# Performance work log

Hardware: AMD Instinct MI355X
Metric: run time of the kernel (lower is better)

## Reference

```python
import jax, jax.numpy as jnp
import numpy as np
import math

B, N, M = 128, 16, 32
D_OBS, D_OUT = 128, 128            # obs_input_dim, obs_output_dim (== obs_output_dim_other)
D_OA, D_AV = 136, 128              # obs_act_input_dim, obs_act_output_dim
D_OBS_O, D_OA_O, D_AV_O = 128, 136, 128
D_FINAL_IN, D_HID, D_FINAL_OUT = 256, 64, 1
N_ACT = 8


def setup_inputs() -> dict:
    key = jax.random.key(0)
    ks = jax.random.split(key, 16)
    s = 0.05
    return {
        "states": jax.random.normal(ks[0], (B, N, D_OBS), jnp.float32),
        "policies": jax.random.uniform(ks[1], (B, N, N_ACT), jnp.float32),
        "actions": jax.random.uniform(ks[2], (B, N, N_ACT), jnp.float32),
        "states_other": jax.random.normal(ks[3], (B, M, D_OBS_O), jnp.float32),
        "actions_other": jax.random.uniform(ks[4], (B, M, N_ACT), jnp.float32),
        # weights stored as [in, out] (torch Linear applies x @ W.T)
        "Wk": jax.random.normal(ks[5], (D_OBS, D_OUT), jnp.float32) * s,
        "Wq": jax.random.normal(ks[6], (D_OBS, D_OUT), jnp.float32) * s,
        "Wv": jax.random.normal(ks[7], (D_OA, D_AV), jnp.float32) * s,
        "Wk_o": jax.random.normal(ks[8], (D_OBS_O, D_OUT), jnp.float32) * s,
        "Wq_o": jax.random.normal(ks[9], (D_OBS, D_OUT), jnp.float32) * s,
        "Wv_o": jax.random.normal(ks[10], (D_OA_O, D_AV_O), jnp.float32) * s,
        "W1": jax.random.normal(ks[11], (D_FINAL_IN, D_HID), jnp.float32) * s,
        "W2": jax.random.normal(ks[12], (D_HID, D_FINAL_OUT), jnp.float32) * s,
    }


def reference(states, policies, actions, states_other, actions_other,
              Wk, Wq, Wv, Wk_o, Wq_o, Wv_o, W1, W2):
    d_k = float(D_OUT)
    d_k_o = float(D_OUT)  # d_k_obs_other = obs_output_dim_other

    obs_actions = jnp.concatenate([states, actions], axis=-1)   # [B,N,D_OA]
    obs_policy = jnp.concatenate([states, policies], axis=-1)   # [B,N,D_OA]

    k = states @ Wk                                             # [B,N,D_OUT]
    q = states @ Wq
    score = jnp.einsum('bid,bjd->bij', q, k)                    # [B,N,N]
    # torch softmaxes over the key axis (after reshape gymnastics)
    weight = jax.nn.softmax(score / math.sqrt(d_k), axis=-1)    # [B,N,N]
    ret_weight = weight

    # oap[b,j,k] = obs_policy[b,k] if j==k else obs_actions[b,k]
    eye = jnp.eye(N, dtype=states.dtype)[None, :, :, None]      # [1,N,N,1]
    oap = eye * obs_policy[:, None, :, :] + (1.0 - eye) * obs_actions[:, None, :, :]  # [B,N,N,D_OA]
    av = jnp.tanh(oap @ Wv)                                     # [B,N(j),N(k),D_AV]

    # torch: repeat av over a new agent axis i, multiply by weight[b,i,k], sum over k
    wav = jnp.einsum('bik,bjkd->bijd', weight, av)              # [B,N,N,D_AV]

    obs_actions_other = jnp.concatenate([states_other, actions_other], axis=-1)  # [B,M,D_OA_O]
    k_o = states_other @ Wk_o                                   # [B,M,D_OUT]
    q_o = states @ Wq_o                                         # [B,N,D_OUT]
    av_o = jnp.tanh(obs_actions_other @ Wv_o)                   # [B,M,D_AV_O]

    score_o = jnp.einsum('bid,bmd->bim', q_o, k_o)              # [B,N,M]
    # torch softmax dim=-2: over the agent axis (faithful, even if unusual)
    weight_o = jax.nn.softmax(score_o / math.sqrt(d_k_o), axis=1)  # [B,N,M]
    wav_o = jnp.einsum('bim,bmd->bid', weight_o, av_o)          # [B,N,D_AV_O]
    wav_o_b = jnp.broadcast_to(wav_o[:, :, None, :], (wav_o.shape[0], N, N, D_AV_O))

    node = jnp.concatenate([wav, wav_o_b], axis=-1)             # [B,N,N,256]
    h = jax.nn.leaky_relu(node @ W1)                            # [B,N,N,64]
    value = h @ W2                                              # [B,N,N,1]
    return value, ret_weight, weight_o[..., None]
```

## Files before the change

### kernel.cpp

```cpp
#include <hip/hip_runtime.h>
#include <math.h>

#define NB   128
#define NN   16
#define MM   32
#define DD   128
#define NACT 8
#define HH   64

#define OFF_G   0
#define OFF_GO  16384
#define OFF_Q   32768
#define OFF_QO  (OFF_Q  + NB*NN*DD)
#define OFF_P   (OFF_QO + NB*NN*DD)
#define OFF_PO  (OFF_P  + NB*NN*HH)
#define OFF_V   (OFF_PO + NB*MM*HH)
#define WS_FLOATS (OFF_V + NB*NN*HH)

__device__ float g_ws[WS_FLOATS];

__launch_bounds__(256)
__global__ void k0_gram(const float* __restrict__ Wq,  const float* __restrict__ Wk,
                        const float* __restrict__ Wqo, const float* __restrict__ Wko) {
    __shared__ float sA[16 * 129];
    __shared__ float sB[16 * 129];
    const int blk = blockIdx.x;
    const int mat = blk >> 6;
    const int tile = blk & 63;
    const int r0 = (tile >> 3) * 16, c0 = (tile & 7) * 16;
    const float* A  = mat ? Wqo : Wq;
    const float* Bm = mat ? Wko : Wk;
    float* outp = g_ws + (mat ? OFF_GO : OFF_G);
    const int t = threadIdx.x;
    for (int idx = t; idx < 16 * 128; idx += 256) {
        int r = idx >> 7, c = idx & 127;
        sA[r * 129 + c] = A [(r0 + r) * 128 + c];
        sB[r * 129 + c] = Bm[(c0 + r) * 128 + c];
    }
    __syncthreads();
    const int r = t >> 4, c = t & 15;
    float acc = 0.f;
    #pragma unroll 8
    for (int o = 0; o < 128; ++o) acc += sA[r * 129 + o] * sB[c * 129 + o];
    outp[(r0 + r) * 128 + (c0 + c)] = acc;
}

#define AVO_P 132
__launch_bounds__(512)
__global__ void k1_proj(const float* __restrict__ states,   const float* __restrict__ policies,
                        const float* __restrict__ actions,  const float* __restrict__ states_o,
                        const float* __restrict__ actions_o,
                        const float* __restrict__ Wv, const float* __restrict__ Wvo,
                        const float* __restrict__ W1) {
    __shared__ float sm[4096 + 256 + 32 * AVO_P];
    const int bs = blockIdx.x >> 1;
    const int side = blockIdx.x & 1;
    const int t = threadIdx.x;

    if (side == 0) {
        float* s_st = sm;
        float* s_ac = sm + 2048;
        float* s_po = sm + 2176;
        float* s_aa = sm + 2304;
        float* s_ap = sm + 4352;
        ((float4*)s_st)[t] = ((const float4*)(states + bs * NN * DD))[t];
        if (t < NN * NACT) {
            s_ac[t] = actions [bs * NN * NACT + t];
            s_po[t] = policies[bs * NN * NACT + t];
        }
        __syncthreads();
        {
            const int g = t >> 7, c = t & 127;
            float q4[4] = {0,0,0,0}, qo4[4] = {0,0,0,0}, av4[4] = {0,0,0,0};
            const float* G  = g_ws + OFF_G;
            const float* Go = g_ws + OFF_GO;
            for (int kk = 0; kk < DD; ++kk) {
                float wg = G[kk * 128 + c], wgo = Go[kk * 128 + c], wv = Wv[kk * 128 + c];
                #pragma unroll
                for (int u = 0; u < 4; ++u) {
                    float x = s_st[(g + 4 * u) * 128 + kk];
                    q4[u] += x * wg; qo4[u] += x * wgo; av4[u] += x * wv;
                }
            }
            float aa[4], ap[4];
            #pragma unroll
            for (int u = 0; u < 4; ++u) { aa[u] = av4[u]; ap[u] = av4[u]; }
            for (int kk = 0; kk < NACT; ++kk) {
                float wv = Wv[(DD + kk) * 128 + c];
                #pragma unroll
                for (int u = 0; u < 4; ++u) {
                    aa[u] += s_ac[(g + 4 * u) * NACT + kk] * wv;
                    ap[u] += s_po[(g + 4 * u) * NACT + kk] * wv;
                }
            }
            #pragma unroll
            for (int u = 0; u < 4; ++u) {
                int row = g + 4 * u;
                g_ws[OFF_Q  + bs * 2048 + row * 128 + c] = q4[u];
                g_ws[OFF_QO + bs * 2048 + row * 128 + c] = qo4[u];
                s_aa[row * 128 + c] = tanhf(aa[u]);
                s_ap[row * 128 + c] = tanhf(ap[u]);
            }
        }
        __syncthreads();
        {
            const int i = t >> 5, h2 = (t & 31) * 2;
            float p0 = 0.f, p1 = 0.f, v0 = 0.f, v1 = 0.f;
            for (int kk = 0; kk < DD; ++kk) {
                float2 w = *(const float2*)(W1 + kk * HH + h2);
                float a = s_aa[i * 128 + kk];
                float d = s_ap[i * 128 + kk] - a;
                p0 += a * w.x; p1 += a * w.y;
                v0 += d * w.x; v1 += d * w.y;
            }
            *(float2*)(g_ws + OFF_P + bs * NN * HH + i * HH + h2) = make_float2(p0, p1);
            *(float2*)(g_ws + OFF_V + bs * NN * HH + i * HH + h2) = make_float2(v0, v1);
        }
    } else {
        float* s_so = sm;
        float* s_ao = sm + 4096;
        float* s_av = sm + 4352;
        ((float4*)s_so)[t]       = ((const float4*)(states_o + bs * MM * DD))[t];
        ((float4*)s_so)[t + 512] = ((const float4*)(states_o + bs * MM * DD))[t + 512];
        if (t < MM * NACT) s_ao[t] = actions_o[bs * MM * NACT + t];
        __syncthreads();
        {
            const int g = t >> 7, c = t & 127;
            float av8[8] = {0,0,0,0,0,0,0,0};
            for (int kk = 0; kk < DD; ++kk) {
                float wvo = Wvo[kk * 128 + c];
                #pragma unroll
                for (int u = 0; u < 8; ++u) av8[u] += s_so[(g + 4 * u) * 128 + kk] * wvo;
            }
            for (int kk = 0; kk < NACT; ++kk) {
                float wvo = Wvo[(DD + kk) * 128 + c];
                #pragma unroll
                for (int u = 0; u < 8; ++u) av8[u] += s_ao[(g + 4 * u) * NACT + kk] * wvo;
            }
            #pragma unroll
            for (int u = 0; u < 8; ++u) s_av[(g + 4 * u) * AVO_P + c] = tanhf(av8[u]);
        }
        __syncthreads();
        {
            const int r = t >> 4, h4 = (t & 15) * 4;
            float4 acc = {0.f, 0.f, 0.f, 0.f};
            for (int kk = 0; kk < DD; ++kk) {
                float4 w = *(const float4*)(W1 + (DD + kk) * HH + h4);
                float a = s_av[r * AVO_P + kk];
                acc.x += a * w.x; acc.y += a * w.y; acc.z += a * w.z; acc.w += a * w.w;
            }
            *(float4*)(g_ws + OFF_PO + bs * MM * HH + r * HH + h4) = acc;
        }
    }
}

__launch_bounds__(512)
__global__ void k2_attn(const float* __restrict__ states, const float* __restrict__ states_o,
                        const float* __restrict__ W2, float* __restrict__ out) {
    __shared__ float s_q [16 * 129];
    __shared__ float s_qo[16 * 129];
    __shared__ float s_st[16 * 129];
    __shared__ float s_so[32 * 129];
    __shared__ float s_P [16 * 64];
    __shared__ float s_Po[32 * 64];
    __shared__ float s_V [16 * 65];
    __shared__ float s_U [16 * 65];
    __shared__ float s_w [16 * 17];
    __shared__ float s_wo[16 * 33];
    __shared__ float s_W2[64];
    const int b = blockIdx.x, t = threadIdx.x;

    for (int idx = t; idx < NN * DD; idx += 512) {
        int r = idx >> 7, d = idx & 127;
        s_q [r * 129 + d] = g_ws[OFF_Q  + b * 2048 + idx];
        s_qo[r * 129 + d] = g_ws[OFF_QO + b * 2048 + idx];
        s_st[r * 129 + d] = states[b * 2048 + idx];
    }
    for (int idx = t; idx < MM * DD; idx += 512) {
        int r = idx >> 7, d = idx & 127;
        s_so[r * 129 + d] = states_o[b * 4096 + idx];
    }
    if (t < 256) ((float4*)s_P)[t] = ((const float4*)(g_ws + OFF_P + b * NN * HH))[t];
    ((float4*)s_Po)[t] = ((const float4*)(g_ws + OFF_PO + b * MM * HH))[t];
    for (int idx = t; idx < NN * HH; idx += 512) {
        int r = idx >> 6, h = idx & 63;
        s_V[r * 65 + h] = g_ws[OFF_V + b * NN * HH + idx];
    }
    if (t < HH) s_W2[t] = W2[t];
    __syncthreads();

    const float scale = 0.08838834764831845f;
    {
        int i = t >> 5, m = t & 31;
        float acc = 0.f;
        #pragma unroll 8
        for (int d = 0; d < DD; ++d) acc += s_qo[i * 129 + d] * s_so[m * 129 + d];
        s_wo[i * 33 + m] = acc * scale;
    }
    if (t < 256) {
        int i = t >> 4, j = t & 15;
        float acc = 0.f;
        #pragma unroll 8
        for (int d = 0; d < DD; ++d) acc += s_q[i * 129 + d] * s_st[j * 129 + d];
        s_w[i * 17 + j] = acc * scale;
    }
    __syncthreads();

    if (t < NN) {
        int i = t;
        float mx = -1e30f;
        #pragma unroll
        for (int j = 0; j < NN; ++j) mx = fmaxf(mx, s_w[i * 17 + j]);
        float e[NN], sum = 0.f;
        #pragma unroll
        for (int j = 0; j < NN; ++j) { e[j] = expf(s_w[i * 17 + j] - mx); sum += e[j]; }
        float inv = 1.f / sum;
        #pragma unroll
        for (int j = 0; j < NN; ++j) s_w[i * 17 + j] = e[j] * inv;
    } else if (t >= 64 && t < 64 + MM) {
        int m = t - 64;
        float mx = -1e30f;
        #pragma unroll
        for (int i = 0; i < NN; ++i) mx = fmaxf(mx, s_wo[i * 33 + m]);
        float e[NN], sum = 0.f;
        #pragma unroll
        for (int i = 0; i < NN; ++i) { e[i] = expf(s_wo[i * 33 + m] - mx); sum += e[i]; }
        float inv = 1.f / sum;
        #pragma unroll
        for (int i = 0; i < NN; ++i) s_wo[i * 33 + m] = e[i] * inv;
    }
    __syncthreads();

    if (t < NN * NN) out[NB * 256 + b * 256 + t] = s_w[(t >> 4) * 17 + (t & 15)];
    out[2 * NB * 256 + b * 512 + t] = s_wo[(t >> 5) * 33 + (t & 31)];

    {
        int i = t >> 5, h2 = (t & 31) * 2;
        float u0 = 0.f, u1 = 0.f;
        #pragma unroll
        for (int k = 0; k < NN; ++k) {
            float w = s_w[i * 17 + k];
            u0 += w * s_P[k * 64 + h2];
            u1 += w * s_P[k * 64 + h2 + 1];
        }
        #pragma unroll
        for (int m = 0; m < MM; ++m) {
            float w = s_wo[i * 33 + m];
            u0 += w * s_Po[m * 64 + h2];
            u1 += w * s_Po[m * 64 + h2 + 1];
        }
        s_U[i * 65 + h2]     = u0;
        s_U[i * 65 + h2 + 1] = u1;
    }
    __syncthreads();

    if (t < NN * NN) {
        int i = t >> 4, j = t & 15;
        float wij = s_w[i * 17 + j];
        float acc = 0.f;
        #pragma unroll
        for (int h = 0; h < HH; ++h) {
            float x = s_U[i * 65 + h] + wij * s_V[j * 65 + h];
            x = (x > 0.f) ? x : 0.01f * x;
            acc += x * s_W2[h];
        }
        out[b * 256 + t] = acc;
    }
}

extern "C" void kernel_launch(void* const* d_in, const int* in_sizes, int n_in,
                              void* d_out, int out_size, void* d_ws, size_t ws_size,
                              hipStream_t stream) {
    const float* states    = (const float*)d_in[0];
    const float* policies  = (const float*)d_in[1];
    const float* actions   = (const float*)d_in[2];
    const float* states_o  = (const float*)d_in[3];
    const float* actions_o = (const float*)d_in[4];
    const float* Wk        = (const float*)d_in[5];
    const float* Wq        = (const float*)d_in[6];
    const float* Wv        = (const float*)d_in[7];
    const float* Wk_o      = (const float*)d_in[8];
    const float* Wq_o      = (const float*)d_in[9];
    const float* Wv_o      = (const float*)d_in[10];
    const float* W1        = (const float*)d_in[11];
    const float* W2        = (const float*)d_in[12];
    float* out = (float*)d_out;

    hipLaunchKernelGGL(k0_gram, dim3(128), dim3(256), 0, stream, Wq, Wk, Wq_o, Wk_o);
    hipLaunchKernelGGL(k1_proj, dim3(256), dim3(512), 0, stream,
                       states, policies, actions, states_o, actions_o, Wv, Wv_o, W1);
    hipLaunchKernelGGL(k2_attn, dim3(128), dim3(512), 0, stream, states, states_o, W2, out);
}
```

Measured before the change: 118.0 us.

## Split projection and attention into row-tiled GEMM kernels with more blocks

Replaces the per-batch projection kernel (256 blocks) with a 32-row-tiled GEMM kernel over flattened rows (1280 blocks), adds a second kernel that does the W1 projections and both attention score matmuls across 768 blocks, and leaves a light final kernel for the softmaxes and value output. The aim is to expose far more parallelism on a GPU with many CUs, where the old 128/256-block grids underfilled the device. In exchange, intermediates (aa, diff, av_o, scores) now round-trip through global memory and there is one extra kernel launch.

```diff
diff --git a/kernel.cpp b/kernel.cpp
--- a/kernel.cpp
+++ b/kernel.cpp
@@ -1,21 +1,26 @@
 #include <hip/hip_runtime.h>
 #include <math.h>
 
-#define NB   128
-#define NN   16
-#define MM   32
-#define DD   128
+#define NB 128
+#define NN 16
+#define MM 32
+#define DD 128
 #define NACT 8
-#define HH   64
+#define HH 64
 
 #define OFF_G   0
 #define OFF_GO  16384
 #define OFF_Q   32768
-#define OFF_QO  (OFF_Q  + NB*NN*DD)
-#define OFF_P   (OFF_QO + NB*NN*DD)
-#define OFF_PO  (OFF_P  + NB*NN*HH)
-#define OFF_V   (OFF_PO + NB*MM*HH)
-#define WS_FLOATS (OFF_V + NB*NN*HH)
+#define OFF_QO  (OFF_Q  + 2048*128)
+#define OFF_AA  (OFF_QO + 2048*128)
+#define OFF_DF  (OFF_AA + 2048*128)
+#define OFF_AVO (OFF_DF + 2048*128)
+#define OFF_P   (OFF_AVO + 4096*128)
+#define OFF_V   (OFF_P  + 2048*64)
+#define OFF_PO  (OFF_V  + 2048*64)
+#define OFF_S   (OFF_PO + 4096*64)
+#define OFF_SO  (OFF_S  + 128*256)
+#define WS_FLOATS (OFF_SO + 128*512)
 
 __device__ float g_ws[WS_FLOATS];
 
@@ -45,222 +50,258 @@
     outp[(r0 + r) * 128 + (c0 + c)] = acc;
 }
 
-#define AVO_P 132
-__launch_bounds__(512)
-__global__ void k1_proj(const float* __restrict__ states,   const float* __restrict__ policies,
-                        const float* __restrict__ actions,  const float* __restrict__ states_o,
-                        const float* __restrict__ actions_o,
-                        const float* __restrict__ Wv, const float* __restrict__ Wvo,
-                        const float* __restrict__ W1) {
-    __shared__ float sm[4096 + 256 + 32 * AVO_P];
-    const int bs = blockIdx.x >> 1;
-    const int side = blockIdx.x & 1;
+__launch_bounds__(256)
+__global__ void k_proj(const float* __restrict__ states,   const float* __restrict__ policies,
+                       const float* __restrict__ actions,  const float* __restrict__ states_o,
+                       const float* __restrict__ actions_o,
+                       const float* __restrict__ Wv, const float* __restrict__ Wvo) {
+    __shared__ float AT[128][34];
+    __shared__ float s_c1[32][NACT];
+    __shared__ float s_c2[32][NACT];
     const int t = threadIdx.x;
-
-    if (side == 0) {
-        float* s_st = sm;
-        float* s_ac = sm + 2048;
-        float* s_po = sm + 2176;
-        float* s_aa = sm + 2304;
-        float* s_ap = sm + 4352;
-        ((float4*)s_st)[t] = ((const float4*)(states + bs * NN * DD))[t];
-        if (t < NN * NACT) {
-            s_ac[t] = actions [bs * NN * NACT + t];
-            s_po[t] = policies[bs * NN * NACT + t];
+    const int tx = t & 15, ty = t >> 4;
+    const int blk = blockIdx.x;
+
+    const float* Asrc; const float* Bsrc; float* dst;
+    int bcol, mode, r0;
+    if (blk < 768) {
+        int rt = blk / 12, ct = blk % 12;
+        r0 = rt * 32;
+        Asrc = states + r0 * 128;
+        if (ct < 4)      { Bsrc = g_ws + OFF_G;  bcol = ct * 32;       dst = g_ws + OFF_Q  + r0 * 128; mode = 0; }
+        else if (ct < 8) { Bsrc = g_ws + OFF_GO; bcol = (ct - 4) * 32; dst = g_ws + OFF_QO + r0 * 128; mode = 0; }
+        else             { Bsrc = Wv;            bcol = (ct - 8) * 32; dst = g_ws + OFF_AA + r0 * 128; mode = 1; }
+    } else {
+        int tile = blk - 768;
+        int rt = tile >> 2, ct = tile & 3;
+        r0 = rt * 32;
+        Asrc = states_o + r0 * 128;
+        Bsrc = Wvo; bcol = ct * 32; dst = g_ws + OFF_AVO + r0 * 128; mode = 2;
+    }
+
+    #pragma unroll
+    for (int u = 0; u < 4; ++u) {
+        int f4 = t + u * 256;
+        int row = f4 >> 5, c4 = (f4 & 31) * 4;
+        float4 v = *(const float4*)(Asrc + row * 128 + c4);
+        AT[c4 + 0][row] = v.x; AT[c4 + 1][row] = v.y;
+        AT[c4 + 2][row] = v.z; AT[c4 + 3][row] = v.w;
+    }
+    {
+        int row = t >> 3, k = t & 7;
+        if (mode == 1) {
+            s_c1[row][k] = actions [(r0 + row) * NACT + k];
+            s_c2[row][k] = policies[(r0 + row) * NACT + k];
+        } else if (mode == 2) {
+            s_c1[row][k] = actions_o[(r0 + row) * NACT + k];
+        }
+    }
+    __syncthreads();
+
+    const int cc = bcol + 2 * tx;
+    float a00 = 0.f, a01 = 0.f, a10 = 0.f, a11 = 0.f;
+    #pragma unroll 8
+    for (int kk = 0; kk < 128; ++kk) {
+        float2 a  = *(const float2*)&AT[kk][2 * ty];
+        float2 bv = *(const float2*)(Bsrc + kk * 128 + cc);
+        a00 += a.x * bv.x; a01 += a.x * bv.y;
+        a10 += a.y * bv.x; a11 += a.y * bv.y;
+    }
+
+    if (mode == 0) {
+        *(float2*)(dst + (2 * ty)     * 128 + cc) = make_float2(a00, a01);
+        *(float2*)(dst + (2 * ty + 1) * 128 + cc) = make_float2(a10, a11);
+    } else if (mode == 1) {
+        float aa00 = a00, aa01 = a01, aa10 = a10, aa11 = a11;
+        float ap00 = a00, ap01 = a01, ap10 = a10, ap11 = a11;
+        #pragma unroll
+        for (int k = 0; k < NACT; ++k) {
+            float2 w = *(const float2*)(Wv + (128 + k) * 128 + cc);
+            float c1a = s_c1[2 * ty][k], c1b = s_c1[2 * ty + 1][k];
+            float c2a = s_c2[2 * ty][k], c2b = s_c2[2 * ty + 1][k];
+            aa00 += c1a * w.x; aa01 += c1a * w.y; aa10 += c1b * w.x; aa11 += c1b * w.y;
+            ap00 += c2a * w.x; ap01 += c2a * w.y; ap10 += c2b * w.x; ap11 += c2b * w.y;
+        }
+        aa00 = tanhf(aa00); aa01 = tanhf(aa01); aa10 = tanhf(aa10); aa11 = tanhf(aa11);
+        ap00 = tanhf(ap00); ap01 = tanhf(ap01); ap10 = tanhf(ap10); ap11 = tanhf(ap11);
+        float* ddf = g_ws + OFF_DF + r0 * 128;
+        *(float2*)(dst + (2 * ty)     * 128 + cc) = make_float2(aa00, aa01);
+        *(float2*)(dst + (2 * ty + 1) * 128 + cc) = make_float2(aa10, aa11);
+        *(float2*)(ddf + (2 * ty)     * 128 + cc) = make_float2(ap00 - aa00, ap01 - aa01);
+        *(float2*)(ddf + (2 * ty + 1) * 128 + cc) = make_float2(ap10 - aa10, ap11 - aa11);
+    } else {
+        #pragma unroll
+        for (int k = 0; k < NACT; ++k) {
+            float2 w = *(const float2*)(Wvo + (128 + k) * 128 + cc);
+            float c1a = s_c1[2 * ty][k], c1b = s_c1[2 * ty + 1][k];
+            a00 += c1a * w.x; a01 += c1a * w.y; a10 += c1b * w.x; a11 += c1b * w.y;
+        }
+        *(float2*)(dst + (2 * ty)     * 128 + cc) = make_float2(tanhf(a00), tanhf(a01));
+        *(float2*)(dst + (2 * ty + 1) * 128 + cc) = make_float2(tanhf(a10), tanhf(a11));
+    }
+}
+
+__launch_bounds__(256)
+__global__ void k_w1(const float* __restrict__ states, const float* __restrict__ states_o,
+                     const float* __restrict__ W1) {
+    __shared__ float smem[6336];
+    const int blk = blockIdx.x, t = threadIdx.x;
+    const float scale = 0.08838834764831845f;
+
+    if (blk < 512) {
+        const int rt = blk >> 1, ct = blk & 1;
+        const int fr = rt * 32;
+        const float* Asrc; const float* Bsrc; float* dst;
+        if (fr < 2048)      { Asrc = g_ws + OFF_AA  + fr * 128;          Bsrc = W1;            dst = g_ws + OFF_P  + fr * 64; }
+        else if (fr < 4096) { Asrc = g_ws + OFF_DF  + (fr - 2048) * 128; Bsrc = W1;            dst = g_ws + OFF_V  + (fr - 2048) * 64; }
+        else                { Asrc = g_ws + OFF_AVO + (fr - 4096) * 128; Bsrc = W1 + 128 * 64; dst = g_ws + OFF_PO + (fr - 4096) * 64; }
+        #pragma unroll
+        for (int u = 0; u < 4; ++u) {
+            int f4 = t + u * 256;
+            int row = f4 >> 5, c4 = (f4 & 31) * 4;
+            float4 v = *(const float4*)(Asrc + row * 128 + c4);
+            smem[(c4 + 0) * 34 + row] = v.x; smem[(c4 + 1) * 34 + row] = v.y;
+            smem[(c4 + 2) * 34 + row] = v.z; smem[(c4 + 3) * 34 + row] = v.w;
         }
         __syncthreads();
-        {
-            const int g = t >> 7, c = t & 127;
-            float q4[4] = {0,0,0,0}, qo4[4] = {0,0,0,0}, av4[4] = {0,0,0,0};
-            const float* G  = g_ws + OFF_G;
-            const float* Go = g_ws + OFF_GO;
-            for (int kk = 0; kk < DD; ++kk) {
-                float wg = G[kk * 128 + c], wgo = Go[kk * 128 + c], wv = Wv[kk * 128 + c];
-                #pragma unroll
-                for (int u = 0; u < 4; ++u) {
-                    float x = s_st[(g + 4 * u) * 128 + kk];
-                    q4[u] += x * wg; qo4[u] += x * wgo; av4[u] += x * wv;
-                }
-            }
-            float aa[4], ap[4];
-            #pragma unroll
-            for (int u = 0; u < 4; ++u) { aa[u] = av4[u]; ap[u] = av4[u]; }
-            for (int kk = 0; kk < NACT; ++kk) {
-                float wv = Wv[(DD + kk) * 128 + c];
-                #pragma unroll
-                for (int u = 0; u < 4; ++u) {
-                    aa[u] += s_ac[(g + 4 * u) * NACT + kk] * wv;
-                    ap[u] += s_po[(g + 4 * u) * NACT + kk] * wv;
-                }
-            }
-            #pragma unroll
-            for (int u = 0; u < 4; ++u) {
-                int row = g + 4 * u;
-                g_ws[OFF_Q  + bs * 2048 + row * 128 + c] = q4[u];
-                g_ws[OFF_QO + bs * 2048 + row * 128 + c] = qo4[u];
-                s_aa[row * 128 + c] = tanhf(aa[u]);
-                s_ap[row * 128 + c] = tanhf(ap[u]);
-            }
+        const int tx = t & 15, ty = t >> 4;
+        const int cc = ct * 32 + 2 * tx;
+        float a00 = 0.f, a01 = 0.f, a10 = 0.f, a11 = 0.f;
+        #pragma unroll 8
+        for (int kk = 0; kk < 128; ++kk) {
+            float2 a  = *(const float2*)&smem[kk * 34 + 2 * ty];
+            float2 bv = *(const float2*)(Bsrc + kk * 64 + cc);
+            a00 += a.x * bv.x; a01 += a.x * bv.y;
+            a10 += a.y * bv.x; a11 += a.y * bv.y;
+        }
+        *(float2*)(dst + (2 * ty)     * 64 + cc) = make_float2(a00, a01);
+        *(float2*)(dst + (2 * ty + 1) * 64 + cc) = make_float2(a10, a11);
+    } else if (blk < 640) {
+        const int b = blk - 512;
+        float* sq  = smem;
+        float* sst = smem + 2112;
+        #pragma unroll
+        for (int u = 0; u < 2; ++u) {
+            int f4 = t + u * 256;
+            int row = f4 >> 5, c4 = (f4 & 31) * 4;
+            *(float4*)&sq [row * 132 + c4] = *(const float4*)(g_ws + OFF_Q + (b * 16 + row) * 128 + c4);
+            *(float4*)&sst[row * 132 + c4] = *(const float4*)(states      + (b * 16 + row) * 128 + c4);
         }
         __syncthreads();
-        {
-            const int i = t >> 5, h2 = (t & 31) * 2;
-            float p0 = 0.f, p1 = 0.f, v0 = 0.f, v1 = 0.f;
-            for (int kk = 0; kk < DD; ++kk) {
-                float2 w = *(const float2*)(W1 + kk * HH + h2);
-                float a = s_aa[i * 128 + kk];
-                float d = s_ap[i * 128 + kk] - a;
-                p0 += a * w.x; p1 += a * w.y;
-                v0 += d * w.x; v1 += d * w.y;
-            }
-            *(float2*)(g_ws + OFF_P + bs * NN * HH + i * HH + h2) = make_float2(p0, p1);
-            *(float2*)(g_ws + OFF_V + bs * NN * HH + i * HH + h2) = make_float2(v0, v1);
-        }
+        const int i = t >> 4, j = t & 15;
+        float acc = 0.f;
+        #pragma unroll 8
+        for (int d = 0; d < 128; ++d) acc += sq[i * 132 + d] * sst[j * 132 + d];
+        g_ws[OFF_S + b * 256 + t] = acc * scale;
     } else {
-        float* s_so = sm;
-        float* s_ao = sm + 4096;
-        float* s_av = sm + 4352;
-        ((float4*)s_so)[t]       = ((const float4*)(states_o + bs * MM * DD))[t];
-        ((float4*)s_so)[t + 512] = ((const float4*)(states_o + bs * MM * DD))[t + 512];
-        if (t < MM * NACT) s_ao[t] = actions_o[bs * MM * NACT + t];
+        const int b = blk - 640;
+        float* sq  = smem;
+        float* sso = smem + 2112;
+        #pragma unroll
+        for (int u = 0; u < 2; ++u) {
+            int f4 = t + u * 256;
+            int row = f4 >> 5, c4 = (f4 & 31) * 4;
+            *(float4*)&sq[row * 132 + c4] = *(const float4*)(g_ws + OFF_QO + (b * 16 + row) * 128 + c4);
+        }
+        #pragma unroll
+        for (int u = 0; u < 4; ++u) {
+            int f4 = t + u * 256;
+            int row = f4 >> 5, c4 = (f4 & 31) * 4;
+            *(float4*)&sso[row * 132 + c4] = *(const float4*)(states_o + (b * 32 + row) * 128 + c4);
+        }
         __syncthreads();
-        {
-            const int g = t >> 7, c = t & 127;
-            float av8[8] = {0,0,0,0,0,0,0,0};
-            for (int kk = 0; kk < DD; ++kk) {
-                float wvo = Wvo[kk * 128 + c];
-                #pragma unroll
-                for (int u = 0; u < 8; ++u) av8[u] += s_so[(g + 4 * u) * 128 + kk] * wvo;
-            }
-            for (int kk = 0; kk < NACT; ++kk) {
-                float wvo = Wvo[(DD + kk) * 128 + c];
-                #pragma unroll
-                for (int u = 0; u < 8; ++u) av8[u] += s_ao[(g + 4 * u) * NACT + kk] * wvo;
-            }
-            #pragma unroll
-            for (int u = 0; u < 8; ++u) s_av[(g + 4 * u) * AVO_P + c] = tanhf(av8[u]);
-        }
-        __syncthreads();
-        {
-            const int r = t >> 4, h4 = (t & 15) * 4;
-            float4 acc = {0.f, 0.f, 0.f, 0.f};
-            for (int kk = 0; kk < DD; ++kk) {
-                float4 w = *(const float4*)(W1 + (DD + kk) * HH + h4);
-                float a = s_av[r * AVO_P + kk];
-                acc.x += a * w.x; acc.y += a * w.y; acc.z += a * w.z; acc.w += a * w.w;
-            }
-            *(float4*)(g_ws + OFF_PO + bs * MM * HH + r * HH + h4) = acc;
-        }
-    }
-}
-
-__launch_bounds__(512)
-__global__ void k2_attn(const float* __restrict__ states, const float* __restrict__ states_o,
-                        const float* __restrict__ W2, float* __restrict__ out) {
-    __shared__ float s_q [16 * 129];
-    __shared__ float s_qo[16 * 129];
-    __shared__ float s_st[16 * 129];
-    __shared__ float s_so[32 * 129];
+        const int m = t & 31, i0 = t >> 5;
+        float acc0 = 0.f, acc1 = 0.f;
+        #pragma unroll 8
+        for (int d = 0; d < 128; ++d) {
+            float s = sso[m * 132 + d];
+            acc0 += sq[i0 * 132 + d] * s;
+            acc1 += sq[(i0 + 8) * 132 + d] * s;
+        }
+        g_ws[OFF_SO + b * 512 + i0 * 32 + m]       = acc0 * scale;
+        g_ws[OFF_SO + b * 512 + (i0 + 8) * 32 + m] = acc1 * scale;
+    }
+}
+
+__launch_bounds__(256)
+__global__ void k2_fin(const float* __restrict__ W2, float* __restrict__ out) {
+    __shared__ float s_w [16][17];
+    __shared__ float s_wo[16][33];
     __shared__ float s_P [16 * 64];
     __shared__ float s_Po[32 * 64];
-    __shared__ float s_V [16 * 65];
-    __shared__ float s_U [16 * 65];
-    __shared__ float s_w [16 * 17];
-    __shared__ float s_wo[16 * 33];
+    __shared__ float s_V [16][65];
+    __shared__ float s_U [16][65];
     __shared__ float s_W2[64];
     const int b = blockIdx.x, t = threadIdx.x;
 
-    for (int idx = t; idx < NN * DD; idx += 512) {
-        int r = idx >> 7, d = idx & 127;
-        s_q [r * 129 + d] = g_ws[OFF_Q  + b * 2048 + idx];
-        s_qo[r * 129 + d] = g_ws[OFF_QO + b * 2048 + idx];
-        s_st[r * 129 + d] = states[b * 2048 + idx];
-    }
-    for (int idx = t; idx < MM * DD; idx += 512) {
-        int r = idx >> 7, d = idx & 127;
-        s_so[r * 129 + d] = states_o[b * 4096 + idx];
-    }
-    if (t < 256) ((float4*)s_P)[t] = ((const float4*)(g_ws + OFF_P + b * NN * HH))[t];
-    ((float4*)s_Po)[t] = ((const float4*)(g_ws + OFF_PO + b * MM * HH))[t];
-    for (int idx = t; idx < NN * HH; idx += 512) {
-        int r = idx >> 6, h = idx & 63;
-        s_V[r * 65 + h] = g_ws[OFF_V + b * NN * HH + idx];
-    }
-    if (t < HH) s_W2[t] = W2[t];
-    __syncthreads();
-
-    const float scale = 0.08838834764831845f;
-    {
-        int i = t >> 5, m = t & 31;
-        float acc = 0.f;
-        #pragma unroll 8
-        for (int d = 0; d < DD; ++d) acc += s_qo[i * 129 + d] * s_so[m * 129 + d];
-        s_wo[i * 33 + m] = acc * scale;
-    }
-    if (t < 256) {
-        int i = t >> 4, j = t & 15;
-        float acc = 0.f;
-        #pragma unroll 8
-        for (int d = 0; d < DD; ++d) acc += s_q[i * 129 + d] * s_st[j * 129 + d];
-        s_w[i * 17 + j] = acc * scale;
-    }
-    __syncthreads();
-
-    if (t < NN) {
-        int i = t;
+    s_w[t >> 4][t & 15] = g_ws[OFF_S + b * 256 + t];
+    s_wo[t >> 5][t & 31]            = g_ws[OFF_SO + b * 512 + t];
+    s_wo[(t + 256) >> 5][t & 31]    = g_ws[OFF_SO + b * 512 + 256 + t];
+    ((float4*)s_P)[t] = ((const float4*)(g_ws + OFF_P + b * 1024))[t];
+    ((float4*)s_Po)[t]       = ((const float4*)(g_ws + OFF_PO + b * 2048))[t];
+    ((float4*)s_Po)[t + 256] = ((const float4*)(g_ws + OFF_PO + b * 2048))[t + 256];
+    #pragma unroll
+    for (int u = 0; u < 4; ++u) {
+        int idx = t + u * 256;
+        s_V[idx >> 6][idx & 63] = g_ws[OFF_V + b * 1024 + idx];
+    }
+    if (t < 64) s_W2[t] = W2[t];
+    __syncthreads();
+
+    if (t < 16) {
         float mx = -1e30f;
         #pragma unroll
-        for (int j = 0; j < NN; ++j) mx = fmaxf(mx, s_w[i * 17 + j]);
+        for (int j = 0; j < NN; ++j) mx = fmaxf(mx, s_w[t][j]);
         float e[NN], sum = 0.f;
         #pragma unroll
-        for (int j = 0; j < NN; ++j) { e[j] = expf(s_w[i * 17 + j] - mx); sum += e[j]; }
+        for (int j = 0; j < NN; ++j) { e[j] = expf(s_w[t][j] - mx); sum += e[j]; }
         float inv = 1.f / sum;
         #pragma unroll
-        for (int j = 0; j < NN; ++j) s_w[i * 17 + j] = e[j] * inv;
-    } else if (t >= 64 && t < 64 + MM) {
+        for (int j = 0; j < NN; ++j) s_w[t][j] = e[j] * inv;
+    } else if (t >= 64 && t < 96) {
         int m = t - 64;
         float mx = -1e30f;
         #pragma unroll
-        for (int i = 0; i < NN; ++i) mx = fmaxf(mx, s_wo[i * 33 + m]);
+        for (int i = 0; i < NN; ++i) mx = fmaxf(mx, s_wo[i][m]);
         float e[NN], sum = 0.f;
         #pragma unroll
-        for (int i = 0; i < NN; ++i) { e[i] = expf(s_wo[i * 33 + m] - mx); sum += e[i]; }
+        for (int i = 0; i < NN; ++i) { e[i] = expf(s_wo[i][m] - mx); sum += e[i]; }
         float inv = 1.f / sum;
         #pragma unroll
-        for (int i = 0; i < NN; ++i) s_wo[i * 33 + m] = e[i] * inv;
-    }
-    __syncthreads();
-
-    if (t < NN * NN) out[NB * 256 + b * 256 + t] = s_w[(t >> 4) * 17 + (t & 15)];
-    out[2 * NB * 256 + b * 512 + t] = s_wo[(t >> 5) * 33 + (t & 31)];
+        for (int i = 0; i < NN; ++i) s_wo[i][m] = e[i] * inv;
+    }
+    __syncthreads();
+
+    out[NB * 256 + b * 256 + t] = s_w[t >> 4][t & 15];
+    out[2 * NB * 256 + b * 512 + t]       = s_wo[t >> 5][t & 31];
+    out[2 * NB * 256 + b * 512 + 256 + t] = s_wo[(t + 256) >> 5][t & 31];
 
     {
-        int i = t >> 5, h2 = (t & 31) * 2;
-        float u0 = 0.f, u1 = 0.f;
+        int i = t >> 4, h0 = (t & 15) * 4;
+        float u0 = 0.f, u1 = 0.f, u2 = 0.f, u3 = 0.f;
         #pragma unroll
         for (int k = 0; k < NN; ++k) {
-            float w = s_w[i * 17 + k];
-            u0 += w * s_P[k * 64 + h2];
-            u1 += w * s_P[k * 64 + h2 + 1];
+            float w = s_w[i][k];
+            float4 p = *(const float4*)&s_P[k * 64 + h0];
+            u0 += w * p.x; u1 += w * p.y; u2 += w * p.z; u3 += w * p.w;
         }
         #pragma unroll
         for (int m = 0; m < MM; ++m) {
-            float w = s_wo[i * 33 + m];
-            u0 += w * s_Po[m * 64 + h2];
-            u1 += w * s_Po[m * 64 + h2 + 1];
-        }
-        s_U[i * 65 + h2]     = u0;
-        s_U[i * 65 + h2 + 1] = u1;
-    }
-    __syncthreads();
-
-    if (t < NN * NN) {
+            float w = s_wo[i][m];
+            float4 p = *(const float4*)&s_Po[m * 64 + h0];
+            u0 += w * p.x; u1 += w * p.y; u2 += w * p.z; u3 += w * p.w;
+        }
+        s_U[i][h0] = u0; s_U[i][h0 + 1] = u1; s_U[i][h0 + 2] = u2; s_U[i][h0 + 3] = u3;
+    }
+    __syncthreads();
+
+    {
         int i = t >> 4, j = t & 15;
-        float wij = s_w[i * 17 + j];
+        float wij = s_w[i][j];
         float acc = 0.f;
         #pragma unroll
         for (int h = 0; h < HH; ++h) {
-            float x = s_U[i * 65 + h] + wij * s_V[j * 65 + h];
+            float x = s_U[i][h] + wij * s_V[j][h];
             x = (x > 0.f) ? x : 0.01f * x;
             acc += x * s_W2[h];
         }
@@ -286,8 +327,9 @@
     const float* W2        = (const float*)d_in[12];
     float* out = (float*)d_out;
 
-    hipLaunchKernelGGL(k0_gram, dim3(128), dim3(256), 0, stream, Wq, Wk, Wq_o, Wk_o);
-    hipLaunchKernelGGL(k1_proj, dim3(256), dim3(512), 0, stream,
-                       states, policies, actions, states_o, actions_o, Wv, Wv_o, W1);
-    hipLaunchKernelGGL(k2_attn, dim3(128), dim3(512), 0, stream, states, states_o, W2, out);
-}
+    hipLaunchKernelGGL(k0_gram, dim3(128),  dim3(256), 0, stream, Wq, Wk, Wq_o, Wk_o);
+    hipLaunchKernelGGL(k_proj,  dim3(1280), dim3(256), 0, stream,
+                       states, policies, actions, states_o, actions_o, Wv, Wv_o);
+    hipLaunchKernelGGL(k_w1,    dim3(768),  dim3(256), 0, stream, states, states_o, W1);
+    hipLaunchKernelGGL(k2_fin,  dim3(128),  dim3(256), 0, stream, W2, out);
+}
```

After: 124.5 us. 5.5% more time.

## Fuse projections and attention per side, drop Gram precompute kernel

Applied to the files above, without the earlier changes.

Replaces the three-kernel pipeline (Gram matrix precompute, projection, attention) with two kernels. The first kernel computes Q, K and V directly on each side (self and other) and finishes attention scores, softmax and the W1 partial products in the same block. The second kernel only combines the partial U and V terms into the final value. This removes one launch, the Gram precompute and the global round trips of Q/Qo and states, and it uses float4 weight loads. In exchange it recomputes K projections per batch instead of folding them into a Gram matrix, and the self and other sides now carry unequal amounts of work.

```diff
diff --git a/kernel.cpp b/kernel.cpp
--- a/kernel.cpp
+++ b/kernel.cpp
@@ -1,271 +1,259 @@
 #include <hip/hip_runtime.h>
 #include <math.h>
 
-#define NB   128
-#define NN   16
-#define MM   32
-#define DD   128
+#define NB 128
+#define NN 16
+#define MM 32
+#define DD 128
 #define NACT 8
-#define HH   64
-
-#define OFF_G   0
-#define OFF_GO  16384
-#define OFF_Q   32768
-#define OFF_QO  (OFF_Q  + NB*NN*DD)
-#define OFF_P   (OFF_QO + NB*NN*DD)
-#define OFF_PO  (OFF_P  + NB*NN*HH)
-#define OFF_V   (OFF_PO + NB*MM*HH)
-#define WS_FLOATS (OFF_V + NB*NN*HH)
+#define HH 64
+
+#define WS_W  0
+#define WS_V  32768
+#define WS_US 163840
+#define WS_UO 294912
+#define WS_FLOATS (WS_UO + 131072)
 
 __device__ float g_ws[WS_FLOATS];
 
-__launch_bounds__(256)
-__global__ void k0_gram(const float* __restrict__ Wq,  const float* __restrict__ Wk,
-                        const float* __restrict__ Wqo, const float* __restrict__ Wko) {
-    __shared__ float sA[16 * 129];
-    __shared__ float sB[16 * 129];
-    const int blk = blockIdx.x;
-    const int mat = blk >> 6;
-    const int tile = blk & 63;
-    const int r0 = (tile >> 3) * 16, c0 = (tile & 7) * 16;
-    const float* A  = mat ? Wqo : Wq;
-    const float* Bm = mat ? Wko : Wk;
-    float* outp = g_ws + (mat ? OFF_GO : OFF_G);
-    const int t = threadIdx.x;
-    for (int idx = t; idx < 16 * 128; idx += 256) {
-        int r = idx >> 7, c = idx & 127;
-        sA[r * 129 + c] = A [(r0 + r) * 128 + c];
-        sB[r * 129 + c] = Bm[(c0 + r) * 128 + c];
-    }
-    __syncthreads();
-    const int r = t >> 4, c = t & 15;
-    float acc = 0.f;
-    #pragma unroll 8
-    for (int o = 0; o < 128; ++o) acc += sA[r * 129 + o] * sB[c * 129 + o];
-    outp[(r0 + r) * 128 + (c0 + c)] = acc;
-}
-
-#define AVO_P 132
-__launch_bounds__(512)
-__global__ void k1_proj(const float* __restrict__ states,   const float* __restrict__ policies,
+#define A_ST 0
+#define A_Q  2112
+#define A_K  4224
+#define A_AA 6336
+#define A_DF 8448
+#define A_P  10560
+#define A_W  11648
+#define A_AC 11920
+#define A_PO 12048
+#define B_ST  0
+#define B_STO 2112
+#define B_QO  6336
+#define B_KOT 8448
+#define B_AVO 12672
+#define B_PO  16896
+#define B_WO  19072
+#define B_AO  19600
+#define SM_FLOATS 19856
+
+__device__ __forceinline__ float4 tanh4(float4 v) {
+    float4 r; r.x = tanhf(v.x); r.y = tanhf(v.y); r.z = tanhf(v.z); r.w = tanhf(v.w); return r;
+}
+__device__ __forceinline__ void fma4(float4& a, float s, const float4& w) {
+    a.x += s * w.x; a.y += s * w.y; a.z += s * w.z; a.w += s * w.w;
+}
+
+__launch_bounds__(512, 1)
+__global__ void k_sides(const float* __restrict__ states,   const float* __restrict__ policies,
                         const float* __restrict__ actions,  const float* __restrict__ states_o,
                         const float* __restrict__ actions_o,
-                        const float* __restrict__ Wv, const float* __restrict__ Wvo,
-                        const float* __restrict__ W1) {
-    __shared__ float sm[4096 + 256 + 32 * AVO_P];
-    const int bs = blockIdx.x >> 1;
+                        const float* __restrict__ Wq,  const float* __restrict__ Wk,
+                        const float* __restrict__ Wv,  const float* __restrict__ Wqo,
+                        const float* __restrict__ Wko, const float* __restrict__ Wvo,
+                        const float* __restrict__ W1,
+                        float* __restrict__ out) {
+    __shared__ float sm[SM_FLOATS];
+    const int b = blockIdx.x >> 1;
     const int side = blockIdx.x & 1;
     const int t = threadIdx.x;
+    const float scale = 0.08838834764831845f;
 
     if (side == 0) {
-        float* s_st = sm;
-        float* s_ac = sm + 2048;
-        float* s_po = sm + 2176;
-        float* s_aa = sm + 2304;
-        float* s_ap = sm + 4352;
-        ((float4*)s_st)[t] = ((const float4*)(states + bs * NN * DD))[t];
-        if (t < NN * NACT) {
-            s_ac[t] = actions [bs * NN * NACT + t];
-            s_po[t] = policies[bs * NN * NACT + t];
-        }
-        __syncthreads();
-        {
-            const int g = t >> 7, c = t & 127;
-            float q4[4] = {0,0,0,0}, qo4[4] = {0,0,0,0}, av4[4] = {0,0,0,0};
-            const float* G  = g_ws + OFF_G;
-            const float* Go = g_ws + OFF_GO;
-            for (int kk = 0; kk < DD; ++kk) {
-                float wg = G[kk * 128 + c], wgo = Go[kk * 128 + c], wv = Wv[kk * 128 + c];
-                #pragma unroll
-                for (int u = 0; u < 4; ++u) {
-                    float x = s_st[(g + 4 * u) * 128 + kk];
-                    q4[u] += x * wg; qo4[u] += x * wgo; av4[u] += x * wv;
-                }
-            }
-            float aa[4], ap[4];
-            #pragma unroll
-            for (int u = 0; u < 4; ++u) { aa[u] = av4[u]; ap[u] = av4[u]; }
+        {
+            int row = t >> 5, c4 = (t & 31) * 4;
+            *(float4*)&sm[A_ST + row * 132 + c4] = *(const float4*)(states + b * 2048 + row * 128 + c4);
+            if (t < 128) sm[A_AC + t] = actions [b * 128 + t];
+            else if (t < 256) sm[A_PO + (t - 128)] = policies[b * 128 + (t - 128)];
+        }
+        __syncthreads();
+        {
+            const int i = t >> 5, c4 = (t & 31) * 4;
+            float4 aq = {0,0,0,0}, ak = {0,0,0,0}, av = {0,0,0,0};
+            #pragma unroll 4
+            for (int kk = 0; kk < DD; ++kk) {
+                float x = sm[A_ST + i * 132 + kk];
+                fma4(aq, x, *(const float4*)(Wq + kk * 128 + c4));
+                fma4(ak, x, *(const float4*)(Wk + kk * 128 + c4));
+                fma4(av, x, *(const float4*)(Wv + kk * 128 + c4));
+            }
+            float4 aa = av, ap = av;
+            #pragma unroll
             for (int kk = 0; kk < NACT; ++kk) {
-                float wv = Wv[(DD + kk) * 128 + c];
-                #pragma unroll
-                for (int u = 0; u < 4; ++u) {
-                    aa[u] += s_ac[(g + 4 * u) * NACT + kk] * wv;
-                    ap[u] += s_po[(g + 4 * u) * NACT + kk] * wv;
-                }
-            }
-            #pragma unroll
-            for (int u = 0; u < 4; ++u) {
-                int row = g + 4 * u;
-                g_ws[OFF_Q  + bs * 2048 + row * 128 + c] = q4[u];
-                g_ws[OFF_QO + bs * 2048 + row * 128 + c] = qo4[u];
-                s_aa[row * 128 + c] = tanhf(aa[u]);
-                s_ap[row * 128 + c] = tanhf(ap[u]);
-            }
-        }
-        __syncthreads();
-        {
-            const int i = t >> 5, h2 = (t & 31) * 2;
-            float p0 = 0.f, p1 = 0.f, v0 = 0.f, v1 = 0.f;
-            for (int kk = 0; kk < DD; ++kk) {
-                float2 w = *(const float2*)(W1 + kk * HH + h2);
-                float a = s_aa[i * 128 + kk];
-                float d = s_ap[i * 128 + kk] - a;
-                p0 += a * w.x; p1 += a * w.y;
-                v0 += d * w.x; v1 += d * w.y;
-            }
-            *(float2*)(g_ws + OFF_P + bs * NN * HH + i * HH + h2) = make_float2(p0, p1);
-            *(float2*)(g_ws + OFF_V + bs * NN * HH + i * HH + h2) = make_float2(v0, v1);
+                float4 wv = *(const float4*)(Wv + (DD + kk) * 128 + c4);
+                fma4(aa, sm[A_AC + i * NACT + kk], wv);
+                fma4(ap, sm[A_PO + i * NACT + kk], wv);
+            }
+            aa = tanh4(aa); ap = tanh4(ap);
+            float4 df; df.x = ap.x - aa.x; df.y = ap.y - aa.y; df.z = ap.z - aa.z; df.w = ap.w - aa.w;
+            *(float4*)&sm[A_Q  + i * 132 + c4] = aq;
+            *(float4*)&sm[A_K  + i * 132 + c4] = ak;
+            *(float4*)&sm[A_AA + i * 132 + c4] = aa;
+            *(float4*)&sm[A_DF + i * 132 + c4] = df;
+        }
+        __syncthreads();
+        if (t < 256) {
+            int i = t >> 4, j = t & 15;
+            float acc = 0.f;
+            #pragma unroll 8
+            for (int d = 0; d < DD; ++d) acc += sm[A_Q + i * 132 + d] * sm[A_K + j * 132 + d];
+            sm[A_W + i * 17 + j] = acc * scale;
+        } else {
+            int tt = t - 256, i = tt >> 4, h4 = (tt & 15) * 4;
+            float4 accp = {0,0,0,0}, accv = {0,0,0,0};
+            #pragma unroll 4
+            for (int kk = 0; kk < DD; ++kk) {
+                float4 w4 = *(const float4*)(W1 + kk * HH + h4);
+                fma4(accp, sm[A_AA + i * 132 + kk], w4);
+                fma4(accv, sm[A_DF + i * 132 + kk], w4);
+            }
+            *(float4*)&sm[A_P + i * 68 + h4] = accp;
+            *(float4*)(g_ws + WS_V + b * 1024 + i * 64 + h4) = accv;
+        }
+        __syncthreads();
+        if (t < NN) {
+            float mx = -1e30f;
+            #pragma unroll
+            for (int j = 0; j < NN; ++j) mx = fmaxf(mx, sm[A_W + t * 17 + j]);
+            float e[NN], sum = 0.f;
+            #pragma unroll
+            for (int j = 0; j < NN; ++j) { e[j] = expf(sm[A_W + t * 17 + j] - mx); sum += e[j]; }
+            float inv = 1.f / sum;
+            #pragma unroll
+            for (int j = 0; j < NN; ++j) sm[A_W + t * 17 + j] = e[j] * inv;
+        }
+        __syncthreads();
+        if (t < 256) {
+            float wv = sm[A_W + (t >> 4) * 17 + (t & 15)];
+            out[NB * 256 + b * 256 + t] = wv;
+            g_ws[WS_W + b * 256 + t] = wv;
+        }
+        {
+            int i = t >> 5, h2 = (t & 31) * 2;
+            float u0 = 0.f, u1 = 0.f;
+            #pragma unroll
+            for (int k = 0; k < NN; ++k) {
+                float wv = sm[A_W + i * 17 + k];
+                u0 += wv * sm[A_P + k * 68 + h2];
+                u1 += wv * sm[A_P + k * 68 + h2 + 1];
+            }
+            *(float2*)(g_ws + WS_US + b * 1024 + i * 64 + h2) = make_float2(u0, u1);
         }
     } else {
-        float* s_so = sm;
-        float* s_ao = sm + 4096;
-        float* s_av = sm + 4352;
-        ((float4*)s_so)[t]       = ((const float4*)(states_o + bs * MM * DD))[t];
-        ((float4*)s_so)[t + 512] = ((const float4*)(states_o + bs * MM * DD))[t + 512];
-        if (t < MM * NACT) s_ao[t] = actions_o[bs * MM * NACT + t];
-        __syncthreads();
-        {
-            const int g = t >> 7, c = t & 127;
-            float av8[8] = {0,0,0,0,0,0,0,0};
-            for (int kk = 0; kk < DD; ++kk) {
-                float wvo = Wvo[kk * 128 + c];
-                #pragma unroll
-                for (int u = 0; u < 8; ++u) av8[u] += s_so[(g + 4 * u) * 128 + kk] * wvo;
-            }
+        {
+            int row = t >> 5, c4 = (t & 31) * 4;
+            *(float4*)&sm[B_ST + row * 132 + c4] = *(const float4*)(states + b * 2048 + row * 128 + c4);
+            int i2 = t + 512, row2 = (i2 >> 5) - 16, c42 = (i2 & 31) * 4;
+            *(float4*)&sm[B_STO + row2 * 132 + c42] = *(const float4*)(states_o + b * 4096 + row2 * 128 + c42);
+            int i3 = t + 1024, row3 = (i3 >> 5) - 32, c43 = (i3 & 31) * 4;
+            *(float4*)&sm[B_STO + (row3 + 16) * 132 + c43] = *(const float4*)(states_o + b * 4096 + (row3 + 16) * 128 + c43);
+            if (t < 256) sm[B_AO + t] = actions_o[b * 256 + t];
+        }
+        __syncthreads();
+        {
+            const int r = t >> 5, c4 = (t & 31) * 4;
+            float4 aqo = {0,0,0,0}, ak0 = {0,0,0,0}, ak1 = {0,0,0,0}, av0 = {0,0,0,0}, av1 = {0,0,0,0};
+            #pragma unroll 2
+            for (int kk = 0; kk < DD; ++kk) {
+                float xs = sm[B_ST  + r * 132 + kk];
+                float x0 = sm[B_STO + r * 132 + kk];
+                float x1 = sm[B_STO + (r + 16) * 132 + kk];
+                float4 wq4 = *(const float4*)(Wqo + kk * 128 + c4);
+                float4 wk4 = *(const float4*)(Wko + kk * 128 + c4);
+                float4 wv4 = *(const float4*)(Wvo + kk * 128 + c4);
+                fma4(aqo, xs, wq4);
+                fma4(ak0, x0, wk4); fma4(ak1, x1, wk4);
+                fma4(av0, x0, wv4); fma4(av1, x1, wv4);
+            }
+            #pragma unroll
             for (int kk = 0; kk < NACT; ++kk) {
-                float wvo = Wvo[(DD + kk) * 128 + c];
-                #pragma unroll
-                for (int u = 0; u < 8; ++u) av8[u] += s_ao[(g + 4 * u) * NACT + kk] * wvo;
-            }
-            #pragma unroll
-            for (int u = 0; u < 8; ++u) s_av[(g + 4 * u) * AVO_P + c] = tanhf(av8[u]);
-        }
-        __syncthreads();
-        {
-            const int r = t >> 4, h4 = (t & 15) * 4;
-            float4 acc = {0.f, 0.f, 0.f, 0.f};
-            for (int kk = 0; kk < DD; ++kk) {
-                float4 w = *(const float4*)(W1 + (DD + kk) * HH + h4);
-                float a = s_av[r * AVO_P + kk];
-                acc.x += a * w.x; acc.y += a * w.y; acc.z += a * w.z; acc.w += a * w.w;
-            }
-            *(float4*)(g_ws + OFF_PO + bs * MM * HH + r * HH + h4) = acc;
+                float4 wv4 = *(const float4*)(Wvo + (DD + kk) * 128 + c4);
+                fma4(av0, sm[B_AO + r * NACT + kk], wv4);
+                fma4(av1, sm[B_AO + (r + 16) * NACT + kk], wv4);
+            }
+            av0 = tanh4(av0); av1 = tanh4(av1);
+            *(float4*)&sm[B_QO  + r * 132 + c4] = aqo;
+            *(float4*)&sm[B_AVO + r * 132 + c4] = av0;
+            *(float4*)&sm[B_AVO + (r + 16) * 132 + c4] = av1;
+            sm[B_KOT + (c4 + 0) * 33 + r] = ak0.x; sm[B_KOT + (c4 + 1) * 33 + r] = ak0.y;
+            sm[B_KOT + (c4 + 2) * 33 + r] = ak0.z; sm[B_KOT + (c4 + 3) * 33 + r] = ak0.w;
+            sm[B_KOT + (c4 + 0) * 33 + r + 16] = ak1.x; sm[B_KOT + (c4 + 1) * 33 + r + 16] = ak1.y;
+            sm[B_KOT + (c4 + 2) * 33 + r + 16] = ak1.z; sm[B_KOT + (c4 + 3) * 33 + r + 16] = ak1.w;
+        }
+        __syncthreads();
+        {
+            int i = t >> 5, m = t & 31;
+            float acc = 0.f;
+            #pragma unroll 8
+            for (int d = 0; d < DD; ++d) acc += sm[B_QO + i * 132 + d] * sm[B_KOT + d * 33 + m];
+            sm[B_WO + i * 33 + m] = acc * scale;
+        }
+        __syncthreads();
+        if (t < MM) {
+            float mx = -1e30f;
+            #pragma unroll
+            for (int i = 0; i < NN; ++i) mx = fmaxf(mx, sm[B_WO + i * 33 + t]);
+            float e[NN], sum = 0.f;
+            #pragma unroll
+            for (int i = 0; i < NN; ++i) { e[i] = expf(sm[B_WO + i * 33 + t] - mx); sum += e[i]; }
+            float inv = 1.f / sum;
+            #pragma unroll
+            for (int i = 0; i < NN; ++i) sm[B_WO + i * 33 + t] = e[i] * inv;
+        }
+        __syncthreads();
+        {
+            int r = t >> 4, h4 = (t & 15) * 4;
+            float4 acc = {0,0,0,0};
+            #pragma unroll 4
+            for (int kk = 0; kk < DD; ++kk) {
+                float4 w4 = *(const float4*)(W1 + (DD + kk) * HH + h4);
+                fma4(acc, sm[B_AVO + r * 132 + kk], w4);
+            }
+            *(float4*)&sm[B_PO + r * 68 + h4] = acc;
+        }
+        __syncthreads();
+        out[2 * NB * 256 + b * 512 + t] = sm[B_WO + (t >> 5) * 33 + (t & 31)];
+        {
+            int i = t >> 5, h2 = (t & 31) * 2;
+            float u0 = 0.f, u1 = 0.f;
+            #pragma unroll
+            for (int m = 0; m < MM; ++m) {
+                float wv = sm[B_WO + i * 33 + m];
+                u0 += wv * sm[B_PO + m * 68 + h2];
+                u1 += wv * sm[B_PO + m * 68 + h2 + 1];
+            }
+            *(float2*)(g_ws + WS_UO + b * 1024 + i * 64 + h2) = make_float2(u0, u1);
         }
     }
 }
 
-__launch_bounds__(512)
-__global__ void k2_attn(const float* __restrict__ states, const float* __restrict__ states_o,
-                        const float* __restrict__ W2, float* __restrict__ out) {
-    __shared__ float s_q [16 * 129];
-    __shared__ float s_qo[16 * 129];
-    __shared__ float s_st[16 * 129];
-    __shared__ float s_so[32 * 129];
-    __shared__ float s_P [16 * 64];
-    __shared__ float s_Po[32 * 64];
-    __shared__ float s_V [16 * 65];
-    __shared__ float s_U [16 * 65];
-    __shared__ float s_w [16 * 17];
-    __shared__ float s_wo[16 * 33];
-    __shared__ float s_W2[64];
+__launch_bounds__(256, 4)
+__global__ void k_fin(const float* __restrict__ W2, float* __restrict__ out) {
+    __shared__ float s_U[16 * 68];
+    __shared__ float s_V[16 * 68];
+    __shared__ float s_w[16 * 17];
+    __shared__ float s_W2[HH];
     const int b = blockIdx.x, t = threadIdx.x;
 
-    for (int idx = t; idx < NN * DD; idx += 512) {
-        int r = idx >> 7, d = idx & 127;
-        s_q [r * 129 + d] = g_ws[OFF_Q  + b * 2048 + idx];
-        s_qo[r * 129 + d] = g_ws[OFF_QO + b * 2048 + idx];
-        s_st[r * 129 + d] = states[b * 2048 + idx];
-    }
-    for (int idx = t; idx < MM * DD; idx += 512) {
-        int r = idx >> 7, d = idx & 127;
-        s_so[r * 129 + d] = states_o[b * 4096 + idx];
-    }
-    if (t < 256) ((float4*)s_P)[t] = ((const float4*)(g_ws + OFF_P + b * NN * HH))[t];
-    ((float4*)s_Po)[t] = ((const float4*)(g_ws + OFF_PO + b * MM * HH))[t];
-    for (int idx = t; idx < NN * HH; idx += 512) {
-        int r = idx >> 6, h = idx & 63;
-        s_V[r * 65 + h] = g_ws[OFF_V + b * NN * HH + idx];
+    s_w[(t >> 4) * 17 + (t & 15)] = g_ws[WS_W + b * 256 + t];
+    #pragma unroll
+    for (int u = 0; u < 4; ++u) {
+        int idx = t + u * 256;
+        int i = idx >> 6, h = idx & 63;
+        s_U[i * 68 + h] = g_ws[WS_US + b * 1024 + idx] + g_ws[WS_UO + b * 1024 + idx];
+        s_V[i * 68 + h] = g_ws[WS_V + b * 1024 + idx];
     }
     if (t < HH) s_W2[t] = W2[t];
     __syncthreads();
 
-    const float scale = 0.08838834764831845f;
-    {
-        int i = t >> 5, m = t & 31;
-        float acc = 0.f;
-        #pragma unroll 8
-        for (int d = 0; d < DD; ++d) acc += s_qo[i * 129 + d] * s_so[m * 129 + d];
-        s_wo[i * 33 + m] = acc * scale;
+    int i = t >> 4, j = t & 15;
+    float wij = s_w[i * 17 + j];
+    float acc = 0.f;
+    #pragma unroll
+    for (int h = 0; h < HH; ++h) {
+        float x = s_U[i * 68 + h] + wij * s_V[j * 68 + h];
+        x = (x > 0.f) ? x : 0.01f * x;
+        acc += x * s_W2[h];
     }
-    if (t < 256) {
-        int i = t >> 4, j = t & 15;
-        float acc = 0.f;
-        #pragma unroll 8
-        for (int d = 0; d < DD; ++d) acc += s_q[i * 129 + d] * s_st[j * 129 + d];
-        s_w[i * 17 + j] = acc * scale;
-    }
-    __syncthreads();
-
-    if (t < NN) {
-        int i = t;
-        float mx = -1e30f;
-        #pragma unroll
-        for (int j = 0; j < NN; ++j) mx = fmaxf(mx, s_w[i * 17 + j]);
-        float e[NN], sum = 0.f;
-        #pragma unroll
-        for (int j = 0; j < NN; ++j) { e[j] = expf(s_w[i * 17 + j] - mx); sum += e[j]; }
-        float inv = 1.f / sum;
-        #pragma unroll
-        for (int j = 0; j < NN; ++j) s_w[i * 17 + j] = e[j] * inv;
-    } else if (t >= 64 && t < 64 + MM) {
-        int m = t - 64;
-        float mx = -1e30f;
-        #pragma unroll
-        for (int i = 0; i < NN; ++i) mx = fmaxf(mx, s_wo[i * 33 + m]);
-        float e[NN], sum = 0.f;
-        #pragma unroll
-        for (int i = 0; i < NN; ++i) { e[i] = expf(s_wo[i * 33 + m] - mx); sum += e[i]; }
-        float inv = 1.f / sum;
-        #pragma unroll
-        for (int i = 0; i < NN; ++i) s_wo[i * 33 + m] = e[i] * inv;
-    }
-    __syncthreads();
-
-    if (t < NN * NN) out[NB * 256 + b * 256 + t] = s_w[(t >> 4) * 17 + (t & 15)];
-    out[2 * NB * 256 + b * 512 + t] = s_wo[(t >> 5) * 33 + (t & 31)];
-
-    {
-        int i = t >> 5, h2 = (t & 31) * 2;
-        float u0 = 0.f, u1 = 0.f;
-        #pragma unroll
-        for (int k = 0; k < NN; ++k) {
-            float w = s_w[i * 17 + k];
-            u0 += w * s_P[k * 64 + h2];
-            u1 += w * s_P[k * 64 + h2 + 1];
-        }
-        #pragma unroll
-        for (int m = 0; m < MM; ++m) {
-            float w = s_wo[i * 33 + m];
-            u0 += w * s_Po[m * 64 + h2];
-            u1 += w * s_Po[m * 64 + h2 + 1];
-        }
-        s_U[i * 65 + h2]     = u0;
-        s_U[i * 65 + h2 + 1] = u1;
-    }
-    __syncthreads();
-
-    if (t < NN * NN) {
-        int i = t >> 4, j = t & 15;
-        float wij = s_w[i * 17 + j];
-        float acc = 0.f;
-        #pragma unroll
-        for (int h = 0; h < HH; ++h) {
-            float x = s_U[i * 65 + h] + wij * s_V[j * 65 + h];
-            x = (x > 0.f) ? x : 0.01f * x;
-            acc += x * s_W2[h];
-        }
-        out[b * 256 + t] = acc;
-    }
+    out[b * 256 + t] = acc;
 }
 
 extern "C" void kernel_launch(void* const* d_in, const int* in_sizes, int n_in,
@@ -286,8 +274,8 @@
     const float* W2        = (const float*)d_in[12];
     float* out = (float*)d_out;
 
-    hipLaunchKernelGGL(k0_gram, dim3(128), dim3(256), 0, stream, Wq, Wk, Wq_o, Wk_o);
-    hipLaunchKernelGGL(k1_proj, dim3(256), dim3(512), 0, stream,
-                       states, policies, actions, states_o, actions_o, Wv, Wv_o, W1);
-    hipLaunchKernelGGL(k2_attn, dim3(128), dim3(512), 0, stream, states, states_o, W2, out);
-}
+    hipLaunchKernelGGL(k_sides, dim3(256), dim3(512), 0, stream,
+                       states, policies, actions, states_o, actions_o,
+                       Wq, Wk, Wv, Wq_o, Wk_o, Wv_o, W1, out);
+    hipLaunchKernelGGL(k_fin, dim3(128), dim3(256), 0, stream, W2, out);
+}
```

Result: no change. 118.2 us (+0.2%).
